# Optimization experiments

Hardware: AMD Instinct MI355X
Metric: run time of the kernel (lower is better)

Reference implementation:

```python
import jax, jax.numpy as jnp
import numpy as np

B, T, C, H, W = 1, 8, 128, 64, 64
F = 64  # num_feat


def setup_inputs() -> dict:
    key = jax.random.key(0)
    ks = jax.random.split(key, 8)
    return {
        "input1": jax.random.normal(ks[0], (B, T, C, H, W), jnp.float32),
        "input2": jax.random.normal(ks[1], (B, T, C, H, W), jnp.float32),
        "W1": jax.random.normal(ks[2], (F, C), jnp.float32) * 0.05,
        "b1": jax.random.normal(ks[3], (F,), jnp.float32) * 0.05,
        "W2": jax.random.normal(ks[4], (F, C), jnp.float32) * 0.05,
        "b2": jax.random.normal(ks[5], (F,), jnp.float32) * 0.05,
        "W3": jax.random.normal(ks[6], (F, C), jnp.float32) * 0.05,
        "b3": jax.random.normal(ks[7], (F,), jnp.float32) * 0.05,
    }


def reference(input1, input2, W1, b1, W2, b2, W3, b3):
    # act == 0 (ReLU branch). Conv1d(kernel=1) == per-position linear projection.
    b, t, c, h, w = input1.shape
    n = h * w
    x1 = input1.reshape(b, t, c, n)  # matches transpose(1,2).reshape then frame slice
    x2 = input2.reshape(b, t, c, n)
    q = jnp.einsum('fc,btcn->btnf', W1, x1) + b1          # [B,T,N,F]
    k = jnp.einsum('fc,btcn->btnf', W2, x2) + b2          # [B,T,N,F]
    g = jnp.einsum('fc,btcn->btnf', W3, x1) + b3          # [B,T,N,F]
    scores = jax.nn.relu(jnp.einsum('btnf,btmf->btnm', q, k))  # [B,T,N,N]
    out = jnp.einsum('btnm,btmf->btnf', scores, g)        # [B,T,N,F]
    # view([B,H,W,F]).permute(0,3,1,2), stacked over T -> [B,T,F,H,W]
    return out.reshape(b, t, h, w, -1).transpose(0, 1, 4, 2, 3)
```

## Files before the change

kernel.cpp:

```cpp
#include <hip/hip_runtime.h>
#include <hip/hip_bf16.h>

constexpr int T = 8;
constexpr int C = 128;
constexpr int N = 4096;
constexpr int F = 64;

typedef __bf16 bf16x8 __attribute__((ext_vector_type(8)));
typedef __bf16 bf16x4 __attribute__((ext_vector_type(4)));
typedef __bf16 bf16x2 __attribute__((ext_vector_type(2)));
typedef float  f32x4  __attribute__((ext_vector_type(4)));
typedef float  f32x16 __attribute__((ext_vector_type(16)));

__global__ __launch_bounds__(256) void setup_kernel(
    const float* __restrict__ W1, const float* __restrict__ W2,
    const float* __restrict__ W3, __bf16* __restrict__ Wb,
    float* __restrict__ out)
{
    int i = blockIdx.x * 256 + threadIdx.x;
    ((f32x4*)out)[i] = (f32x4){0.f, 0.f, 0.f, 0.f};
    if (i < 3 * F * C) {
        int p = i >> 13, r = i & 8191;
        const float* W = (p == 0) ? W1 : (p == 1) ? W2 : W3;
        Wb[i] = (__bf16)W[r];
    }
}

__global__ __launch_bounds__(256) void proj_kernel(
    const float* __restrict__ x1, const float* __restrict__ x2,
    const __bf16* __restrict__ Wb,
    const float* __restrict__ b1, const float* __restrict__ b2,
    const float* __restrict__ b3,
    __bf16* __restrict__ Qb, __bf16* __restrict__ Kb, __bf16* __restrict__ Gw)
{
    const int t  = blockIdx.x >> 6;
    const int nb = blockIdx.x & 63;
    const int n0 = nb * 64;

    constexpr int XS = 136;
    __shared__ __bf16 Xt1[64 * XS];
    __shared__ __bf16 Xt2[64 * XS];

    const int tid = threadIdx.x;
    const int ng  = tid & 15;
    const int cgi = tid >> 4;

#pragma unroll
    for (int pass = 0; pass < 2; ++pass) {
        const int c0 = cgi * 4 + pass * 64;
        const size_t base = ((size_t)t * C + c0) * (size_t)N + n0 + ng * 4;
        f32x4 v1[4], v2[4];
#pragma unroll
        for (int i = 0; i < 4; ++i) {
            v1[i] = *(const f32x4*)&x1[base + (size_t)i * N];
            v2[i] = *(const f32x4*)&x2[base + (size_t)i * N];
        }
#pragma unroll
        for (int j = 0; j < 4; ++j) {
            bf16x4 o1, o2;
#pragma unroll
            for (int i = 0; i < 4; ++i) {
                o1[i] = (__bf16)v1[i][j];
                o2[i] = (__bf16)v2[i][j];
            }
            *(bf16x4*)&Xt1[(ng * 4 + j) * XS + c0] = o1;
            *(bf16x4*)&Xt2[(ng * 4 + j) * XS + c0] = o2;
        }
    }
    __syncthreads();

    const int wave = tid >> 6, lane = tid & 63;
    const int quad = lane >> 4, l16 = lane & 15;

    bf16x8 a1[4], a2[4];
#pragma unroll
    for (int cc = 0; cc < 4; ++cc) {
        a1[cc] = *(const bf16x8*)&Xt1[(wave * 16 + l16) * XS + cc * 32 + quad * 8];
        a2[cc] = *(const bf16x8*)&Xt2[(wave * 16 + l16) * XS + cc * 32 + quad * 8];
    }

#pragma unroll
    for (int p = 0; p < 2; ++p) {
        const __bf16* W    = Wb + (size_t)p * F * C;
        const float*  bias = p ? b2 : b1;
        __bf16*       O    = p ? Kb : Qb;

        f32x4 acc[4];
#pragma unroll
        for (int ft = 0; ft < 4; ++ft) acc[ft] = (f32x4){0.f, 0.f, 0.f, 0.f};
#pragma unroll
        for (int cc = 0; cc < 4; ++cc) {
#pragma unroll
            for (int ft = 0; ft < 4; ++ft) {
                bf16x8 wf = *(const bf16x8*)&W[(ft * 16 + l16) * C + cc * 32 + quad * 8];
                bf16x8 xf = p ? a2[cc] : a1[cc];
                acc[ft] = __builtin_amdgcn_mfma_f32_16x16x32_bf16(wf, xf, acc[ft], 0, 0, 0);
            }
        }
        const int n = n0 + wave * 16 + l16;
#pragma unroll
        for (int ft = 0; ft < 4; ++ft) {
            const int f0 = ft * 16 + quad * 4;
            f32x4 bv = *(const f32x4*)&bias[f0];
            bf16x4 o;
#pragma unroll
            for (int r = 0; r < 4; ++r) o[r] = (__bf16)(acc[ft][r] + bv[r]);
            *(bf16x4*)&O[((size_t)t * N + n) * F + f0] = o;
        }
    }

    {
        const __bf16* W3b = Wb + (size_t)2 * F * C;
        f32x4 acc[4];
#pragma unroll
        for (int ft = 0; ft < 4; ++ft) acc[ft] = (f32x4){0.f, 0.f, 0.f, 0.f};
#pragma unroll
        for (int cc = 0; cc < 4; ++cc) {
#pragma unroll
            for (int ft = 0; ft < 4; ++ft) {
                bf16x8 wf = *(const bf16x8*)&W3b[(ft * 16 + l16) * C + cc * 32 + quad * 8];
                acc[ft] = __builtin_amdgcn_mfma_f32_16x16x32_bf16(a1[cc], wf, acc[ft], 0, 0, 0);
            }
        }
        const int nr0 = n0 + wave * 16 + quad * 4;
#pragma unroll
        for (int ft = 0; ft < 4; ++ft) {
            const int f = ft * 16 + l16;
            const float bv = b3[f];
            bf16x4 o;
#pragma unroll
            for (int r = 0; r < 4; ++r) o[r] = (__bf16)(acc[ft][r] + bv);
            *(bf16x4*)&Gw[((size_t)t * F + f) * (size_t)N + nr0] = o;
        }
    }
}

constexpr int KSPLIT = 4;

__global__ __launch_bounds__(256) void attn_kernel(
    const __bf16* __restrict__ Qb, const __bf16* __restrict__ Kb,
    const __bf16* __restrict__ Gw, float* __restrict__ out)
{
    const int ks = blockIdx.x & (KSPLIT - 1);
    const int qb = (blockIdx.x / KSPLIT) & 31;
    const int t  = blockIdx.x / (KSPLIT * 32);
    const int q0 = qb * 128;

    constexpr int KS = 72;
    __shared__ __bf16 Kt[64 * KS];
    __shared__ __bf16 Gt[64 * KS];

    const int tid = threadIdx.x, wave = tid >> 6, lane = tid & 63;
    const int m32 = lane & 31, hi = lane >> 5;

    bf16x8 qf[4];
    {
        const __bf16* qrow = &Qb[((size_t)t * N + q0 + wave * 32 + m32) * F + hi * 8];
#pragma unroll
        for (int fc = 0; fc < 4; ++fc)
            qf[fc] = *(const bf16x8*)(qrow + fc * 16);
    }

    f32x16 oacc[2];
#pragma unroll
    for (int ft = 0; ft < 2; ++ft)
#pragma unroll
        for (int r = 0; r < 16; ++r) oacc[ft][r] = 0.f;

    const int kb_lo = ks * (N / 64 / KSPLIT);
    const int kb_hi = kb_lo + (N / 64 / KSPLIT);

    const int r8a = tid >> 3,          c8a = (tid & 7) * 8;
    const int r8b = (tid + 256) >> 3,  c8b = c8a;

    bf16x8 kv0, kv1, gv0, gv1;
    {
        const int k0 = kb_lo * 64;
        kv0 = *(const bf16x8*)&Kb[((size_t)t * N + k0 + r8a) * F + c8a];
        kv1 = *(const bf16x8*)&Kb[((size_t)t * N + k0 + r8b) * F + c8b];
        gv0 = *(const bf16x8*)&Gw[((size_t)t * F + r8a) * (size_t)N + k0 + c8a];
        gv1 = *(const bf16x8*)&Gw[((size_t)t * F + r8b) * (size_t)N + k0 + c8b];
    }

    for (int kb = kb_lo; kb < kb_hi; ++kb) {
        __syncthreads();
        *(bf16x8*)&Kt[r8a * KS + c8a] = kv0;
        *(bf16x8*)&Kt[r8b * KS + c8b] = kv1;
        *(bf16x8*)&Gt[r8a * KS + c8a] = gv0;
        *(bf16x8*)&Gt[r8b * KS + c8b] = gv1;
        __syncthreads();

        if (kb + 1 < kb_hi) {
            const int k0 = (kb + 1) * 64;
            kv0 = *(const bf16x8*)&Kb[((size_t)t * N + k0 + r8a) * F + c8a];
            kv1 = *(const bf16x8*)&Kb[((size_t)t * N + k0 + r8b) * F + c8b];
            gv0 = *(const bf16x8*)&Gw[((size_t)t * F + r8a) * (size_t)N + k0 + c8a];
            gv1 = *(const bf16x8*)&Gw[((size_t)t * F + r8b) * (size_t)N + k0 + c8b];
        }

        bf16x8 ps[4];
#pragma unroll
        for (int kt = 0; kt < 2; ++kt) {
            f32x16 s;
#pragma unroll
            for (int r = 0; r < 16; ++r) s[r] = 0.f;
#pragma unroll
            for (int fc = 0; fc < 4; ++fc) {
                bf16x8 kf = *(const bf16x8*)&Kt[(kt * 32 + m32) * KS + fc * 16 + hi * 8];
                s = __builtin_amdgcn_mfma_f32_32x32x16_bf16(kf, qf[fc], s, 0, 0, 0);
            }
            unsigned P[8];
#pragma unroll
            for (int m = 0; m < 8; ++m) {
                union { bf16x2 h; unsigned u; } pk;
                pk.h[0] = (__bf16)fmaxf(s[2 * m], 0.f);
                pk.h[1] = (__bf16)fmaxf(s[2 * m + 1], 0.f);
                P[m] = pk.u;
            }
            asm("v_permlane32_swap_b32 %0, %1" : "+v"(P[0]), "+v"(P[2]));
            asm("v_permlane32_swap_b32 %0, %1" : "+v"(P[1]), "+v"(P[3]));
            asm("v_permlane32_swap_b32 %0, %1" : "+v"(P[4]), "+v"(P[6]));
            asm("v_permlane32_swap_b32 %0, %1" : "+v"(P[5]), "+v"(P[7]));
            union { unsigned u[4]; bf16x8 v; } lo, hiu;
            lo.u[0]  = P[0]; lo.u[1]  = P[1]; lo.u[2]  = P[2]; lo.u[3]  = P[3];
            hiu.u[0] = P[4]; hiu.u[1] = P[5]; hiu.u[2] = P[6]; hiu.u[3] = P[7];
            ps[kt * 2]     = lo.v;
            ps[kt * 2 + 1] = hiu.v;
        }

#pragma unroll
        for (int ft = 0; ft < 2; ++ft)
#pragma unroll
            for (int kt = 0; kt < 2; ++kt)
#pragma unroll
                for (int kc = 0; kc < 2; ++kc) {
                    bf16x8 gfr = *(const bf16x8*)&Gt[(ft * 32 + m32) * KS +
                                                     kt * 32 + kc * 16 + hi * 8];
                    oacc[ft] = __builtin_amdgcn_mfma_f32_32x32x16_bf16(
                        gfr, ps[kt * 2 + kc], oacc[ft], 0, 0, 0);
                }
    }

    const int q = q0 + wave * 32 + m32;
#pragma unroll
    for (int ft = 0; ft < 2; ++ft)
#pragma unroll
        for (int r = 0; r < 16; ++r) {
            int f = ft * 32 + (r & 3) + 8 * (r >> 2) + 4 * hi;
            unsafeAtomicAdd(&out[((size_t)t * F + f) * (size_t)N + q], oacc[ft][r]);
        }
}

extern "C" void kernel_launch(void* const* d_in, const int* in_sizes, int n_in,
                              void* d_out, int out_size, void* d_ws, size_t ws_size,
                              hipStream_t stream) {
    const float* x1 = (const float*)d_in[0];
    const float* x2 = (const float*)d_in[1];
    const float* W1 = (const float*)d_in[2];
    const float* b1 = (const float*)d_in[3];
    const float* W2 = (const float*)d_in[4];
    const float* b2 = (const float*)d_in[5];
    const float* W3 = (const float*)d_in[6];
    const float* b3 = (const float*)d_in[7];
    float* out = (float*)d_out;

    __bf16* Qb = (__bf16*)d_ws;
    __bf16* Kb = Qb + (size_t)T * N * F;
    __bf16* Gw = Kb + (size_t)T * N * F;
    __bf16* Wb = Gw + (size_t)T * N * F;

    setup_kernel<<<dim3(T * F * N / 4 / 256), dim3(256), 0, stream>>>(
        W1, W2, W3, Wb, out);
    proj_kernel<<<dim3(T * (N / 64)), dim3(256), 0, stream>>>(
        x1, x2, Wb, b1, b2, b3, Qb, Kb, Gw);
    attn_kernel<<<dim3(T * 32 * KSPLIT), dim3(256), 0, stream>>>(Qb, Kb, Gw, out);
}
```

Baseline: 151.9 us.

## Split projection across grid.y, double attention K-split, add MFMA priority hints

```diff
diff --git a/kernel.cpp b/kernel.cpp
--- a/kernel.cpp
+++ b/kernel.cpp
@@ -33,13 +33,15 @@
     const float* __restrict__ b3,
     __bf16* __restrict__ Qb, __bf16* __restrict__ Kb, __bf16* __restrict__ Gw)
 {
+    const int pj = blockIdx.y;
     const int t  = blockIdx.x >> 6;
     const int nb = blockIdx.x & 63;
     const int n0 = nb * 64;
 
     constexpr int XS = 136;
-    __shared__ __bf16 Xt1[64 * XS];
-    __shared__ __bf16 Xt2[64 * XS];
+    __shared__ __bf16 Xt[64 * XS];
+
+    const float* X = (pj == 1) ? x2 : x1;
 
     const int tid = threadIdx.x;
     const int ng  = tid & 15;
@@ -49,22 +51,16 @@
     for (int pass = 0; pass < 2; ++pass) {
         const int c0 = cgi * 4 + pass * 64;
         const size_t base = ((size_t)t * C + c0) * (size_t)N + n0 + ng * 4;
-        f32x4 v1[4], v2[4];
-#pragma unroll
-        for (int i = 0; i < 4; ++i) {
-            v1[i] = *(const f32x4*)&x1[base + (size_t)i * N];
-            v2[i] = *(const f32x4*)&x2[base + (size_t)i * N];
-        }
+        f32x4 v[4];
+#pragma unroll
+        for (int i = 0; i < 4; ++i)
+            v[i] = *(const f32x4*)&X[base + (size_t)i * N];
 #pragma unroll
         for (int j = 0; j < 4; ++j) {
-            bf16x4 o1, o2;
-#pragma unroll
-            for (int i = 0; i < 4; ++i) {
-                o1[i] = (__bf16)v1[i][j];
-                o2[i] = (__bf16)v2[i][j];
-            }
-            *(bf16x4*)&Xt1[(ng * 4 + j) * XS + c0] = o1;
-            *(bf16x4*)&Xt2[(ng * 4 + j) * XS + c0] = o2;
+            bf16x4 o;
+#pragma unroll
+            for (int i = 0; i < 4; ++i) o[i] = (__bf16)v[i][j];
+            *(bf16x4*)&Xt[(ng * 4 + j) * XS + c0] = o;
         }
     }
     __syncthreads();
@@ -72,18 +68,16 @@
     const int wave = tid >> 6, lane = tid & 63;
     const int quad = lane >> 4, l16 = lane & 15;
 
-    bf16x8 a1[4], a2[4];
-#pragma unroll
-    for (int cc = 0; cc < 4; ++cc) {
-        a1[cc] = *(const bf16x8*)&Xt1[(wave * 16 + l16) * XS + cc * 32 + quad * 8];
-        a2[cc] = *(const bf16x8*)&Xt2[(wave * 16 + l16) * XS + cc * 32 + quad * 8];
-    }
-
-#pragma unroll
-    for (int p = 0; p < 2; ++p) {
-        const __bf16* W    = Wb + (size_t)p * F * C;
-        const float*  bias = p ? b2 : b1;
-        __bf16*       O    = p ? Kb : Qb;
+    bf16x8 a[4];
+#pragma unroll
+    for (int cc = 0; cc < 4; ++cc)
+        a[cc] = *(const bf16x8*)&Xt[(wave * 16 + l16) * XS + cc * 32 + quad * 8];
+
+    const __bf16* W = Wb + (size_t)pj * F * C;
+
+    if (pj < 2) {
+        const float* bias = pj ? b2 : b1;
+        __bf16*      O    = pj ? Kb : Qb;
 
         f32x4 acc[4];
 #pragma unroll
@@ -93,8 +87,7 @@
 #pragma unroll
             for (int ft = 0; ft < 4; ++ft) {
                 bf16x8 wf = *(const bf16x8*)&W[(ft * 16 + l16) * C + cc * 32 + quad * 8];
-                bf16x8 xf = p ? a2[cc] : a1[cc];
-                acc[ft] = __builtin_amdgcn_mfma_f32_16x16x32_bf16(wf, xf, acc[ft], 0, 0, 0);
+                acc[ft] = __builtin_amdgcn_mfma_f32_16x16x32_bf16(wf, a[cc], acc[ft], 0, 0, 0);
             }
         }
         const int n = n0 + wave * 16 + l16;
@@ -107,10 +100,7 @@
             for (int r = 0; r < 4; ++r) o[r] = (__bf16)(acc[ft][r] + bv[r]);
             *(bf16x4*)&O[((size_t)t * N + n) * F + f0] = o;
         }
-    }
-
-    {
-        const __bf16* W3b = Wb + (size_t)2 * F * C;
+    } else {
         f32x4 acc[4];
 #pragma unroll
         for (int ft = 0; ft < 4; ++ft) acc[ft] = (f32x4){0.f, 0.f, 0.f, 0.f};
@@ -118,8 +108,8 @@
         for (int cc = 0; cc < 4; ++cc) {
 #pragma unroll
             for (int ft = 0; ft < 4; ++ft) {
-                bf16x8 wf = *(const bf16x8*)&W3b[(ft * 16 + l16) * C + cc * 32 + quad * 8];
-                acc[ft] = __builtin_amdgcn_mfma_f32_16x16x32_bf16(a1[cc], wf, acc[ft], 0, 0, 0);
+                bf16x8 wf = *(const bf16x8*)&W[(ft * 16 + l16) * C + cc * 32 + quad * 8];
+                acc[ft] = __builtin_amdgcn_mfma_f32_16x16x32_bf16(a[cc], wf, acc[ft], 0, 0, 0);
             }
         }
         const int nr0 = n0 + wave * 16 + quad * 4;
@@ -135,7 +125,7 @@
     }
 }
 
-constexpr int KSPLIT = 4;
+constexpr int KSPLIT = 8;
 
 __global__ __launch_bounds__(256) void attn_kernel(
     const __bf16* __restrict__ Qb, const __bf16* __restrict__ Kb,
@@ -204,11 +194,13 @@
             f32x16 s;
 #pragma unroll
             for (int r = 0; r < 16; ++r) s[r] = 0.f;
+            __builtin_amdgcn_s_setprio(1);
 #pragma unroll
             for (int fc = 0; fc < 4; ++fc) {
                 bf16x8 kf = *(const bf16x8*)&Kt[(kt * 32 + m32) * KS + fc * 16 + hi * 8];
                 s = __builtin_amdgcn_mfma_f32_32x32x16_bf16(kf, qf[fc], s, 0, 0, 0);
             }
+            __builtin_amdgcn_s_setprio(0);
             unsigned P[8];
 #pragma unroll
             for (int m = 0; m < 8; ++m) {
@@ -228,6 +220,7 @@
             ps[kt * 2 + 1] = hiu.v;
         }
 
+        __builtin_amdgcn_s_setprio(1);
 #pragma unroll
         for (int ft = 0; ft < 2; ++ft)
 #pragma unroll
@@ -239,6 +232,7 @@
                     oacc[ft] = __builtin_amdgcn_mfma_f32_32x32x16_bf16(
                         gfr, ps[kt * 2 + kc], oacc[ft], 0, 0, 0);
                 }
+        __builtin_amdgcn_s_setprio(0);
     }
 
     const int q = q0 + wave * 32 + m32;
@@ -271,7 +265,7 @@
 
     setup_kernel<<<dim3(T * F * N / 4 / 256), dim3(256), 0, stream>>>(
         W1, W2, W3, Wb, out);
-    proj_kernel<<<dim3(T * (N / 64)), dim3(256), 0, stream>>>(
+    proj_kernel<<<dim3(T * (N / 64), 3), dim3(256), 0, stream>>>(
         x1, x2, Wb, b1, b2, b3, Qb, Kb, Gw);
     attn_kernel<<<dim3(T * 32 * KSPLIT), dim3(256), 0, stream>>>(Qb, Kb, Gw, out);
 }
```

Result: slower. 168.8 us (+11.1%).
